# Kernel tuning notes

Measured on AMD Instinct MI355X. Metric: run time of the kernel, lower is better.

The kernel has to match this reference:

```python
import jax, jax.numpy as jnp
import numpy as np

N, E, B, D = 50000, 1600000, 256, 64


def _lin(k, fan_in, fan_out):
    kw, kb = jax.random.split(k)
    bound = 1.0 / np.sqrt(fan_in)
    w = jax.random.uniform(kw, (fan_in, fan_out), jnp.float32, -bound, bound)
    b = jax.random.uniform(kb, (fan_out,), jnp.float32, -bound, bound)
    return w, b


def setup_inputs() -> dict:
    key = jax.random.key(0)
    ks = jax.random.split(key, 16)
    inp = {
        "x": jax.random.normal(ks[0], (N, D), jnp.float32),
        "edge_attr": jax.random.normal(ks[1], (E, D), jnp.float32),
        "u": jax.random.normal(ks[2], (B, D), jnp.float32),
        "edge_index": jax.random.randint(ks[3], (2, E), 0, N, jnp.int32),
        "batch": jnp.sort(jax.random.randint(ks[4], (N,), 0, B, jnp.int32)),
    }
    # three MLPs: edge (in 4D), node (in 3D), global (in 3D); dims [2D, 2D, D]
    specs = [("e", 4 * D), ("n", 3 * D), ("g", 3 * D)]
    ki = 5
    for name, in_dim in specs:
        dims = [in_dim, 2 * D, 2 * D, D]
        for li in range(3):
            w, b = _lin(ks[ki], dims[li], dims[li + 1]); ki += 1
            inp[f"{name}w{li+1}"] = w
            inp[f"{name}b{li+1}"] = b
    return inp


def _mlp(h, w1, b1, w2, b2, w3, b3):
    h = h @ w1 + b1
    h = jax.nn.relu(h) @ w2 + b2
    h = jax.nn.relu(h) @ w3 + b3
    return h


def _scatter_mean(src, idx, num_segments):
    s = jax.ops.segment_sum(src, idx, num_segments=num_segments)
    c = jax.ops.segment_sum(jnp.ones_like(src[:, :1]), idx, num_segments=num_segments)
    return s / jnp.maximum(c, 1.0)


def reference(x, edge_attr, u,
              ew1, eb1, ew2, eb2, ew3, eb3,
              nw1, nb1, nw2, nb2, nw3, nb3,
              gw1, gb1, gw2, gb2, gw3, gb3,
              edge_index, batch):
    row, col = edge_index[0], edge_index[1]
    # edge model: cat[src, dest, edge_attr, u[batch[row]]] -> MLP
    e_in = jnp.concatenate([x[row], x[col], edge_attr, u[batch[row]]], axis=1)  # [E, 4D]
    e = _mlp(e_in, ew1, eb1, ew2, eb2, ew3, eb3)  # [E, D]
    # node model: scatter_mean(edge_attr', row) cat x cat u[batch] -> MLP
    n_agg = _scatter_mean(e, row, x.shape[0])  # [N, D]
    n_in = jnp.concatenate([n_agg, x, u[batch]], axis=1)  # [N, 3D]
    xn = _mlp(n_in, nw1, nb1, nw2, nb2, nw3, nb3)  # [N, D]
    # global model: cat[u, scatter_mean(x', batch), scatter_mean(e', batch[row])]
    edge_mean = _scatter_mean(e, batch[row], u.shape[0])  # [B, D]
    node_mean = _scatter_mean(xn, batch, u.shape[0])  # [B, D]
    g_in = jnp.concatenate([u, node_mean, edge_mean], axis=1)  # [B, 3D]
    un = _mlp(g_in, gw1, gb1, gw2, gb2, gw3, gb3)  # [B, D]
    return xn, e, un
```

## Files before the change

kernel.cpp:

```cpp
#include <hip/hip_runtime.h>

#define NN 50000
#define EE 1600000
#define BBATCH 256
#define DD 64

typedef _Float16 f16;
typedef _Float16 f16x4 __attribute__((ext_vector_type(4)));
typedef _Float16 f16x8 __attribute__((ext_vector_type(8)));
typedef float f32x4 __attribute__((ext_vector_type(4)));

#define MFMA16(a,b,c) __builtin_amdgcn_mfma_f32_16x16x32_f16((a),(b),(c),0,0,0)

constexpr int EW1_RL  = 264;
constexpr int EW1_OFF = 0;
constexpr int EW2_OFF = EW1_OFF + 128 * EW1_RL;
constexpr int EW3_OFF = EW2_OFF + 128 * 136;
constexpr int EH_OFF  = EW3_OFF + 64 * 136;
constexpr int EB_OFF  = EH_OFF + 8 * 16 * 72;
constexpr int ELDS    = EB_OFF + 640;

constexpr int NW1_RL  = 200;
constexpr int NW1_OFF = 0;
constexpr int NW2_OFF = NW1_OFF + 128 * NW1_RL;
constexpr int NW3_OFF = NW2_OFF + 128 * 136;
constexpr int NH_OFF  = NW3_OFF + 64 * 136;
constexpr int NB_OFF  = NH_OFF + 4 * 32 * 136;
constexpr int NLDS    = NB_OFF + 640;

__device__ __forceinline__ f16x8 pack8(const float* __restrict__ p) {
  f32x4 a = *(const f32x4*)p;
  f32x4 b = *(const f32x4*)(p + 4);
  f16x8 r;
  r[0]=(f16)a[0]; r[1]=(f16)a[1]; r[2]=(f16)a[2]; r[3]=(f16)a[3];
  r[4]=(f16)b[0]; r[5]=(f16)b[1]; r[6]=(f16)b[2]; r[7]=(f16)b[3];
  return r;
}
__device__ __forceinline__ f16x8 pack8s(const float* __restrict__ p, float sc) {
  f32x4 a = *(const f32x4*)p;
  f32x4 b = *(const f32x4*)(p + 4);
  a = a * sc; b = b * sc;
  f16x8 r;
  r[0]=(f16)a[0]; r[1]=(f16)a[1]; r[2]=(f16)a[2]; r[3]=(f16)a[3];
  r[4]=(f16)b[0]; r[5]=(f16)b[1]; r[6]=(f16)b[2]; r[7]=(f16)b[3];
  return r;
}
__device__ __forceinline__ f16x8 cvt8(f32x4 a, f32x4 b) {
  f16x8 r;
  r[0]=(f16)a[0]; r[1]=(f16)a[1]; r[2]=(f16)a[2]; r[3]=(f16)a[3];
  r[4]=(f16)b[0]; r[5]=(f16)b[1]; r[6]=(f16)b[2]; r[7]=(f16)b[3];
  return r;
}

template<int KSL, int W1RL, int W1O, int W2O, int W3O>
__device__ __forceinline__ void mlp3_core(f16* __restrict__ sm,
    const float* __restrict__ b1l, const float* __restrict__ b2l,
    const float* __restrict__ b3l,
    const f16x8 (&A1)[2][KSL], const int hb, const int r15, const int g,
    f32x4 (&acc3)[2][4])
{
  #pragma unroll
  for (int hh = 0; hh < 2; ++hh) {
    f32x4 acc[2][4];
    #pragma unroll
    for (int nt = 0; nt < 4; ++nt) {
      const float bv = b1l[(hh*4 + nt)*16 + r15];
      acc[0][nt] = (f32x4){bv, bv, bv, bv};
      acc[1][nt] = acc[0][nt];
    }
    #pragma unroll
    for (int s = 0; s < KSL; ++s) {
      #pragma unroll
      for (int nt = 0; nt < 4; ++nt) {
        const f16x8 bf = *(const f16x8*)&sm[W1O + ((hh*4+nt)*16 + r15) * W1RL + s*32 + g*8];
        acc[0][nt] = MFMA16(A1[0][s], bf, acc[0][nt]);
        acc[1][nt] = MFMA16(A1[1][s], bf, acc[1][nt]);
      }
    }
    #pragma unroll
    for (int mt = 0; mt < 2; ++mt)
      #pragma unroll
      for (int nt = 0; nt < 4; ++nt)
        #pragma unroll
        for (int i = 0; i < 4; ++i)
          sm[hb + (mt*16 + g*4 + i)*136 + (hh*4+nt)*16 + r15] =
              (f16)fmaxf(acc[mt][nt][i], 0.f);
  }

  f16x8 A2[2][4];
  #pragma unroll
  for (int mt = 0; mt < 2; ++mt)
    #pragma unroll
    for (int s = 0; s < 4; ++s)
      A2[mt][s] = *(const f16x8*)&sm[hb + (mt*16 + r15)*136 + s*32 + g*8];

  #pragma unroll
  for (int hh = 0; hh < 2; ++hh) {
    f32x4 acc[2][4];
    #pragma unroll
    for (int nt = 0; nt < 4; ++nt) {
      const float bv = b2l[(hh*4 + nt)*16 + r15];
      acc[0][nt] = (f32x4){bv, bv, bv, bv};
      acc[1][nt] = acc[0][nt];
    }
    #pragma unroll
    for (int s = 0; s < 4; ++s) {
      #pragma unroll
      for (int nt = 0; nt < 4; ++nt) {
        const f16x8 bf = *(const f16x8*)&sm[W2O + ((hh*4+nt)*16 + r15)*136 + s*32 + g*8];
        acc[0][nt] = MFMA16(A2[0][s], bf, acc[0][nt]);
        acc[1][nt] = MFMA16(A2[1][s], bf, acc[1][nt]);
      }
    }
    #pragma unroll
    for (int mt = 0; mt < 2; ++mt)
      #pragma unroll
      for (int nt = 0; nt < 4; ++nt)
        #pragma unroll
        for (int i = 0; i < 4; ++i)
          sm[hb + (mt*16 + g*4 + i)*136 + (hh*4+nt)*16 + r15] =
              (f16)fmaxf(acc[mt][nt][i], 0.f);
  }

  f16x8 A3[2][4];
  #pragma unroll
  for (int mt = 0; mt < 2; ++mt)
    #pragma unroll
    for (int s = 0; s < 4; ++s)
      A3[mt][s] = *(const f16x8*)&sm[hb + (mt*16 + r15)*136 + s*32 + g*8];

  #pragma unroll
  for (int nt = 0; nt < 4; ++nt) {
    const float bv = b3l[nt*16 + r15];
    acc3[0][nt] = (f32x4){bv, bv, bv, bv};
    acc3[1][nt] = acc3[0][nt];
  }
  #pragma unroll
  for (int s = 0; s < 4; ++s) {
    #pragma unroll
    for (int nt = 0; nt < 4; ++nt) {
      const f16x8 bf = *(const f16x8*)&sm[W3O + (nt*16 + r15)*136 + s*32 + g*8];
      acc3[0][nt] = MFMA16(A3[0][s], bf, acc3[0][nt]);
      acc3[1][nt] = MFMA16(A3[1][s], bf, acc3[1][nt]);
    }
  }
}

__global__ void prep_kernel(
    const float* __restrict__ e1, const float* __restrict__ e2, const float* __restrict__ e3,
    const float* __restrict__ n1, const float* __restrict__ n2, const float* __restrict__ n3,
    const float* __restrict__ q1, const float* __restrict__ q2, const float* __restrict__ q3,
    f16* __restrict__ wdst,
    const float* __restrict__ x, const float* __restrict__ u,
    f16* __restrict__ xh, f16* __restrict__ uh,
    const int* __restrict__ ei, int* __restrict__ deg,
    const int* __restrict__ batch, int* __restrict__ bstart)
{
  const int tid = blockIdx.x * 256 + threadIdx.x;

  {
    const int o1=32768,o2=49152,o3=57344,o4=81920,o5=98304,o6=106496,o7=131072,o8=147456,o9=155648;
    if (tid < o9) {
      const float* src; int in, od, rel;
      if      (tid < o1) { src=e1; in=256; od=128; rel=tid;    }
      else if (tid < o2) { src=e2; in=128; od=128; rel=tid-o1; }
      else if (tid < o3) { src=e3; in=128; od=64;  rel=tid-o2; }
      else if (tid < o4) { src=n1; in=192; od=128; rel=tid-o3; }
      else if (tid < o5) { src=n2; in=128; od=128; rel=tid-o4; }
      else if (tid < o6) { src=n3; in=128; od=64;  rel=tid-o5; }
      else if (tid < o7) { src=q1; in=192; od=128; rel=tid-o6; }
      else if (tid < o8) { src=q2; in=128; od=128; rel=tid-o7; }
      else               { src=q3; in=128; od=64;  rel=tid-o8; }
      int o = rel / in, i = rel - o * in;
      wdst[tid] = (f16)src[(size_t)i * od + o];
    }
  }

  if (tid < NN * 64 / 4) {
    f32x4 v = *(const f32x4*)&x[(size_t)tid * 4];
    f16x4 h; h[0]=(f16)v[0]; h[1]=(f16)v[1]; h[2]=(f16)v[2]; h[3]=(f16)v[3];
    *(f16x4*)&xh[(size_t)tid * 4] = h;
  }
  if (tid < BBATCH * 64 / 4) {
    f32x4 v = *(const f32x4*)&u[(size_t)tid * 4];
    f16x4 h; h[0]=(f16)v[0]; h[1]=(f16)v[1]; h[2]=(f16)v[2]; h[3]=(f16)v[3];
    *(f16x4*)&uh[(size_t)tid * 4] = h;
  }

  if (tid < EE) atomicAdd(&deg[ei[tid]], 1);

  if (tid < NN) {
    int b = batch[tid];
    if (tid == 0) { for (int k = 0; k <= b; ++k) bstart[k] = 0; }
    else { int pb = batch[tid - 1]; for (int k = pb + 1; k <= b; ++k) bstart[k] = tid; }
    if (tid == NN - 1) { for (int k = b + 1; k <= BBATCH; ++k) bstart[k] = NN; }
  }
}

__global__ __launch_bounds__(1024) void scan_kernel(const int* __restrict__ deg,
                                                    int* __restrict__ offs,
                                                    int* __restrict__ cursor) {
  const int t = threadIdx.x;
  const int per = (NN + 1023) / 1024;
  const int s0 = t * per;
  int s1 = s0 + per; if (s1 > NN) s1 = NN;
  int sum = 0;
  for (int i = s0; i < s1; ++i) sum += deg[i];
  const int lane = t & 63, wid = t >> 6;
  int v = sum;
  #pragma unroll
  for (int off = 1; off < 64; off <<= 1) {
    int o = __shfl_up(v, off);
    if (lane >= off) v += o;
  }
  __shared__ int wsums[16];
  __shared__ int wexcl[16];
  if (lane == 63) wsums[wid] = v;
  __syncthreads();
  if (t == 0) { int run = 0; for (int k = 0; k < 16; ++k) { wexcl[k] = run; run += wsums[k]; } }
  __syncthreads();
  int run = wexcl[wid] + v - sum;
  for (int i = s0; i < s1; ++i) { int d = deg[i]; offs[i] = run; cursor[i] = run; run += d; }
  if (t == 1023) offs[NN] = run;
}

__global__ void fill_kernel(const int* __restrict__ ei, int* __restrict__ cursor,
                            int* __restrict__ elist) {
  int tid = blockIdx.x * 256 + threadIdx.x;
  if (tid < EE) {
    int r = ei[tid];
    int pos = atomicAdd(&cursor[r], 1);
    elist[pos] = tid;
  }
}

__global__ __launch_bounds__(512, 2) void edge_mlp_kernel(
    const f16* __restrict__ xh, const float* __restrict__ ea,
    const f16* __restrict__ uh, const int* __restrict__ ei,
    const int* __restrict__ batch,
    const f16* __restrict__ w1t, const f16* __restrict__ w2t, const f16* __restrict__ w3t,
    const float* __restrict__ b1, const float* __restrict__ b2, const float* __restrict__ b3,
    float* __restrict__ e_out)
{
  __shared__ __align__(16) f16 sm[ELDS];
  const int t = threadIdx.x;
  for (int c = t; c < 4096; c += 512) { int r = c >> 5, kc = c & 31;
    *(uint4*)&sm[EW1_OFF + r*EW1_RL + kc*8] = *(const uint4*)&w1t[r*256 + kc*8]; }
  for (int c = t; c < 2048; c += 512) { int r = c >> 4, kc = c & 15;
    *(uint4*)&sm[EW2_OFF + r*136 + kc*8] = *(const uint4*)&w2t[r*128 + kc*8]; }
  for (int c = t; c < 1024; c += 512) { int r = c >> 4, kc = c & 15;
    *(uint4*)&sm[EW3_OFF + r*136 + kc*8] = *(const uint4*)&w3t[r*128 + kc*8]; }
  float* bias = (float*)&sm[EB_OFF];
  if (t < 128) { bias[t] = b1[t]; bias[128 + t] = b2[t]; }
  else if (t < 192) { bias[256 + (t - 128)] = b3[t - 128]; }
  __syncthreads();

  const int l = t & 63, w = t >> 6;
  const int r15 = l & 15, g = l >> 4;
  const int hb = EH_OFF + w * (16 * 72);
  const int NT = EE / 256;
  const int stride = gridDim.x;
  const int t0 = blockIdx.x;

  int rC[2], cC[2], bC[2];
  int rN[2], cN[2], bN[2];
  f16x8 Bx[2][6];
  f32x4 Gea[2][2][2];

  auto issueXU = [&](const int (&rr)[2], const int (&cc)[2], const int (&bb)[2]) {
    #pragma unroll
    for (int mt = 0; mt < 2; ++mt) {
      const f16* pr = xh + (size_t)rr[mt] * 64 + g * 8;
      const f16* pc = xh + (size_t)cc[mt] * 64 + g * 8;
      const f16* pu = uh + (size_t)bb[mt] * 64 + g * 8;
      Bx[mt][0] = *(const f16x8*)pr;        Bx[mt][1] = *(const f16x8*)(pr + 32);
      Bx[mt][2] = *(const f16x8*)pc;        Bx[mt][3] = *(const f16x8*)(pc + 32);
      Bx[mt][4] = *(const f16x8*)pu;        Bx[mt][5] = *(const f16x8*)(pu + 32);
    }
  };
  auto issueEA = [&](int tt) {
    #pragma unroll
    for (int mt = 0; mt < 2; ++mt) {
      const float* pe = ea + ((size_t)(tt * 256 + w * 32 + mt * 16 + r15)) * 64 + g * 8;
      #pragma unroll
      for (int ss = 0; ss < 2; ++ss) {
        Gea[mt][ss][0] = *(const f32x4*)(pe + ss * 32);
        Gea[mt][ss][1] = *(const f32x4*)(pe + ss * 32 + 4);
      }
    }
  };

  {
    int rr[2], cc[2], bb[2];
    #pragma unroll
    for (int mt = 0; mt < 2; ++mt) {
      const int eid = t0 * 256 + w * 32 + mt * 16 + r15;
      rr[mt] = ei[eid]; cc[mt] = ei[EE + eid];
    }
    #pragma unroll
    for (int mt = 0; mt < 2; ++mt) bb[mt] = batch[rr[mt]];
    issueXU(rr, cc, bb); issueEA(t0);
    int t1 = t0 + stride; if (t1 >= NT) t1 = t0;
    #pragma unroll
    for (int mt = 0; mt < 2; ++mt) {
      const int eid = t1 * 256 + w * 32 + mt * 16 + r15;
      rC[mt] = ei[eid]; cC[mt] = ei[EE + eid];
    }
    #pragma unroll
    for (int mt = 0; mt < 2; ++mt) bC[mt] = batch[rC[mt]];
  }

  for (int tile = t0; tile < NT; tile += stride) {
    f16x8 A[2][8];
    #pragma unroll
    for (int mt = 0; mt < 2; ++mt) {
      A[mt][0] = Bx[mt][0]; A[mt][1] = Bx[mt][1];
      A[mt][2] = Bx[mt][2]; A[mt][3] = Bx[mt][3];
      A[mt][4] = cvt8(Gea[mt][0][0], Gea[mt][0][1]);
      A[mt][5] = cvt8(Gea[mt][1][0], Gea[mt][1][1]);
      A[mt][6] = Bx[mt][4]; A[mt][7] = Bx[mt][5];
    }

    int t2 = tile + 2 * stride; if (t2 >= NT) t2 = t0;
    #pragma unroll
    for (int mt = 0; mt < 2; ++mt) {
      const int eid = t2 * 256 + w * 32 + mt * 16 + r15;
      rN[mt] = ei[eid]; cN[mt] = ei[EE + eid];
    }

    f32x4 acc1[2][8];
    #pragma unroll
    for (int a = 0; a < 8; ++a) {
      const f32x4 bv = *(const f32x4*)&bias[a*16 + g*4];
      acc1[0][a] = bv; acc1[1][a] = bv;
    }
    #pragma unroll
    for (int s = 0; s < 8; ++s)
      #pragma unroll
      for (int a = 0; a < 8; ++a) {
        const f16x8 wf = *(const f16x8*)&sm[EW1_OFF + (a*16 + r15)*EW1_RL + s*32 + g*8];
        acc1[0][a] = MFMA16(wf, A[0][s], acc1[0][a]);
        acc1[1][a] = MFMA16(wf, A[1][s], acc1[1][a]);
      }

    #pragma unroll
    for (int mt = 0; mt < 2; ++mt) bN[mt] = batch[rN[mt]];

    f16x8 B2[2][4];
    #pragma unroll
    for (int mt = 0; mt < 2; ++mt)
      #pragma unroll
      for (int hh = 0; hh < 2; ++hh) {
        #pragma unroll
        for (int ap = 0; ap < 4; ++ap) {
          const f32x4 v = acc1[mt][hh*4 + ap];
          f16x4 hv;
          hv[0]=(f16)fmaxf(v[0],0.f); hv[1]=(f16)fmaxf(v[1],0.f);
          hv[2]=(f16)fmaxf(v[2],0.f); hv[3]=(f16)fmaxf(v[3],0.f);
          *(f16x4*)&sm[hb + r15*72 + ap*16 + g*4] = hv;
        }
        #pragma unroll
        for (int sl = 0; sl < 2; ++sl)
          B2[mt][hh*2 + sl] = *(const f16x8*)&sm[hb + r15*72 + sl*32 + g*8];
      }

    int t1 = tile + stride; if (t1 >= NT) t1 = t0;
    issueXU(rC, cC, bC);

    f32x4 acc2[2][8];
    #pragma unroll
    for (int a = 0; a < 8; ++a) {
      const f32x4 bv = *(const f32x4*)&bias[128 + a*16 + g*4];
      acc2[0][a] = bv; acc2[1][a] = bv;
    }
    #pragma unroll
    for (int s = 0; s < 4; ++s)
      #pragma unroll
      for (int a = 0; a < 8; ++a) {
        const f16x8 wf = *(const f16x8*)&sm[EW2_OFF + (a*16 + r15)*136 + s*32 + g*8];
        acc2[0][a] = MFMA16(wf, B2[0][s], acc2[0][a]);
        acc2[1][a] = MFMA16(wf, B2[1][s], acc2[1][a]);
      }

    f16x8 B3[2][4];
    #pragma unroll
    for (int mt = 0; mt < 2; ++mt)
      #pragma unroll
      for (int hh = 0; hh < 2; ++hh) {
        #pragma unroll
        for (int ap = 0; ap < 4; ++ap) {
          const f32x4 v = acc2[mt][hh*4 + ap];
          f16x4 hv;
          hv[0]=(f16)fmaxf(v[0],0.f); hv[1]=(f16)fmaxf(v[1],0.f);
          hv[2]=(f16)fmaxf(v[2],0.f); hv[3]=(f16)fmaxf(v[3],0.f);
          *(f16x4*)&sm[hb + r15*72 + ap*16 + g*4] = hv;
        }
        #pragma unroll
        for (int sl = 0; sl < 2; ++sl)
          B3[mt][hh*2 + sl] = *(const f16x8*)&sm[hb + r15*72 + sl*32 + g*8];
      }

    issueEA(t1);

    f32x4 acc3[2][4];
    #pragma unroll
    for (int a = 0; a < 4; ++a) {
      const f32x4 bv = *(const f32x4*)&bias[256 + a*16 + g*4];
      acc3[0][a] = bv; acc3[1][a] = bv;
    }
    #pragma unroll
    for (int s = 0; s < 4; ++s)
      #pragma unroll
      for (int a = 0; a < 4; ++a) {
        const f16x8 wf = *(const f16x8*)&sm[EW3_OFF + (a*16 + r15)*136 + s*32 + g*8];
        acc3[0][a] = MFMA16(wf, B3[0][s], acc3[0][a]);
        acc3[1][a] = MFMA16(wf, B3[1][s], acc3[1][a]);
      }

    const int base = tile * 256 + w * 32;
    #pragma unroll
    for (int mt = 0; mt < 2; ++mt) {
      const int m = base + mt * 16 + r15;
      #pragma unroll
      for (int a = 0; a < 4; ++a)
        *(f32x4*)&e_out[(size_t)m * 64 + a*16 + g*4] = acc3[mt][a];
    }

    #pragma unroll
    for (int mt = 0; mt < 2; ++mt) { rC[mt] = rN[mt]; cC[mt] = cN[mt]; bC[mt] = bN[mt]; }
  }
}

__global__ void nsum_kernel(const float* __restrict__ e_src, const int* __restrict__ offs,
                            const int* __restrict__ elist, float* __restrict__ n_sum) {
  const int l = threadIdx.x & 63;
  const int wid = (blockIdx.x * blockDim.x + threadIdx.x) >> 6;
  const int nw = (gridDim.x * blockDim.x) >> 6;
  for (int node = wid; node < NN; node += nw) {
    const int s = offs[node], e = offs[node + 1];
    float acc = 0.f;
    int j = s;
    for (; j + 16 <= e; j += 16) {
      float v[16];
      #pragma unroll
      for (int k = 0; k < 16; ++k) v[k] = e_src[(size_t)elist[j + k] * 64 + l];
      float s0 = ((v[0]+v[1])+(v[2]+v[3])) + ((v[4]+v[5])+(v[6]+v[7]));
      float s1 = ((v[8]+v[9])+(v[10]+v[11])) + ((v[12]+v[13])+(v[14]+v[15]));
      acc += s0 + s1;
    }
    for (; j + 4 <= e; j += 4) {
      float v0 = e_src[(size_t)elist[j]   * 64 + l];
      float v1 = e_src[(size_t)elist[j+1] * 64 + l];
      float v2 = e_src[(size_t)elist[j+2] * 64 + l];
      float v3 = e_src[(size_t)elist[j+3] * 64 + l];
      acc += (v0 + v1) + (v2 + v3);
    }
    for (; j < e; ++j) acc += e_src[(size_t)elist[j] * 64 + l];
    n_sum[(size_t)node * 64 + l] = acc;
  }
}

__global__ __launch_bounds__(256, 1) void node_mlp_kernel(
    const float* __restrict__ x, const float* __restrict__ u,
    const int* __restrict__ batch, const float* __restrict__ n_sum,
    const int* __restrict__ deg,
    const f16* __restrict__ w1t, const f16* __restrict__ w2t, const f16* __restrict__ w3t,
    const float* __restrict__ b1, const float* __restrict__ b2, const float* __restrict__ b3,
    float* __restrict__ xn_out)
{
  __shared__ __align__(16) f16 sm[NLDS];
  const int t = threadIdx.x;
  for (int c = t; c < 3072; c += 256) { int r = c / 24, kc = c - r * 24;
    *(uint4*)&sm[NW1_OFF + r*NW1_RL + kc*8] = *(const uint4*)&w1t[r*192 + kc*8]; }
  for (int c = t; c < 2048; c += 256) { int r = c >> 4, kc = c & 15;
    *(uint4*)&sm[NW2_OFF + r*136 + kc*8] = *(const uint4*)&w2t[r*128 + kc*8]; }
  for (int c = t; c < 1024; c += 256) { int r = c >> 4, kc = c & 15;
    *(uint4*)&sm[NW3_OFF + r*136 + kc*8] = *(const uint4*)&w3t[r*128 + kc*8]; }
  float* bias = (float*)&sm[NB_OFF];
  if (t < 128) { bias[t] = b1[t]; bias[128 + t] = b2[t]; }
  if (t < 64)  { bias[256 + t] = b3[t]; }
  __syncthreads();

  const int l = t & 63, w = t >> 6;
  const int r15 = l & 15, g = l >> 4;
  const int hb = NH_OFF + w * (32 * 136);
  const int NTT = (NN + 127) / 128;

  for (int tile = blockIdx.x; tile < NTT; tile += gridDim.x) {
    const int base = tile * 128 + w * 32;
    f16x8 A1[2][6];
    #pragma unroll
    for (int mt = 0; mt < 2; ++mt) {
      int raw = base + mt * 16 + r15;
      int node = raw < NN ? raw : NN - 1;
      float inv = 1.0f / fmaxf((float)deg[node], 1.0f);
      const float* sA = n_sum + (size_t)node * 64;
      const float* sB = x + (size_t)node * 64;
      const float* sC = u + (size_t)batch[node] * 64;
      #pragma unroll
      for (int s = 0; s < 6; ++s) {
        const int off = (s & 1) * 32 + g * 8;
        if (s < 2)      A1[mt][s] = pack8s(sA + off, inv);
        else if (s < 4) A1[mt][s] = pack8(sB + off);
        else            A1[mt][s] = pack8(sC + off);
      }
    }
    f32x4 acc3[2][4];
    mlp3_core<6, NW1_RL, NW1_OFF, NW2_OFF, NW3_OFF>(sm, bias, bias + 128, bias + 256,
                                                    A1, hb, r15, g, acc3);
    #pragma unroll
    for (int mt = 0; mt < 2; ++mt)
      #pragma unroll
      for (int nt = 0; nt < 4; ++nt)
        #pragma unroll
        for (int i = 0; i < 4; ++i) {
          const int m = base + mt * 16 + g * 4 + i;
          if (m < NN) xn_out[(size_t)m * 64 + nt * 16 + r15] = acc3[mt][nt][i];
        }
  }
}

__global__ void batch_sum_kernel(const float* __restrict__ xn, const float* __restrict__ n_sum,
                                 const int* __restrict__ deg, const int* __restrict__ bstart,
                                 float* __restrict__ nbsum, float* __restrict__ ebsum,
                                 int* __restrict__ ncnt, int* __restrict__ ecnt) {
  __shared__ float red0[256];
  __shared__ float red1[256];
  __shared__ int   redi[256];
  const int b = blockIdx.x;
  const int s = bstart[b], e = bstart[b + 1];
  const int t = threadIdx.x, c = t & 63, j0 = t >> 6;
  float xs = 0.f, ns = 0.f; int dc = 0;
  for (int j = s + j0; j < e; j += 4) {
    xs += xn[(size_t)j * 64 + c];
    ns += n_sum[(size_t)j * 64 + c];
    if (c == 0) dc += deg[j];
  }
  red0[t] = xs; red1[t] = ns; redi[t] = dc;
  __syncthreads();
  if (t < 128) { red0[t] += red0[t + 128]; red1[t] += red1[t + 128]; redi[t] += redi[t + 128]; }
  __syncthreads();
  if (t < 64) {
    float a0 = red0[t] + red0[t + 64];
    float a1 = red1[t] + red1[t + 64];
    nbsum[b * 64 + t] = a0;
    ebsum[b * 64 + t] = a1;
    if (t == 0) { ncnt[b] = e - s; ecnt[b] = redi[0] + redi[64]; }
  }
}

__global__ __launch_bounds__(256, 1) void global_mlp_kernel(
    const float* __restrict__ u, const float* __restrict__ nbsum,
    const float* __restrict__ ebsum, const int* __restrict__ ncnt,
    const int* __restrict__ ecnt,
    const f16* __restrict__ w1t, const f16* __restrict__ w2t, const f16* __restrict__ w3t,
    const float* __restrict__ b1, const float* __restrict__ b2, const float* __restrict__ b3,
    float* __restrict__ un_out)
{
  __shared__ __align__(16) f16 sm[NLDS];
  const int t = threadIdx.x;
  for (int c = t; c < 3072; c += 256) { int r = c / 24, kc = c - r * 24;
    *(uint4*)&sm[NW1_OFF + r*NW1_RL + kc*8] = *(const uint4*)&w1t[r*192 + kc*8]; }
  for (int c = t; c < 2048; c += 256) { int r = c >> 4, kc = c & 15;
    *(uint4*)&sm[NW2_OFF + r*136 + kc*8] = *(const uint4*)&w2t[r*128 + kc*8]; }
  for (int c = t; c < 1024; c += 256) { int r = c >> 4, kc = c & 15;
    *(uint4*)&sm[NW3_OFF + r*136 + kc*8] = *(const uint4*)&w3t[r*128 + kc*8]; }
  float* bias = (float*)&sm[NB_OFF];
  if (t < 128) { bias[t] = b1[t]; bias[128 + t] = b2[t]; }
  if (t < 64)  { bias[256 + t] = b3[t]; }
  __syncthreads();

  const int l = t & 63, w = t >> 6;
  const int r15 = l & 15, g = l >> 4;
  const int hb = NH_OFF + w * (32 * 136);
  const int base = blockIdx.x * 128 + w * 32;

  f16x8 A1[2][6];
  #pragma unroll
  for (int mt = 0; mt < 2; ++mt) {
    const int r = base + mt * 16 + r15;
    const float invn = 1.0f / fmaxf((float)ncnt[r], 1.0f);
    const float inve = 1.0f / fmaxf((float)ecnt[r], 1.0f);
    const float* sA = u + (size_t)r * 64;
    const float* sB = nbsum + (size_t)r * 64;
    const float* sC = ebsum + (size_t)r * 64;
    #pragma unroll
    for (int s = 0; s < 6; ++s) {
      const int off = (s & 1) * 32 + g * 8;
      if (s < 2)      A1[mt][s] = pack8(sA + off);
      else if (s < 4) A1[mt][s] = pack8s(sB + off, invn);
      else            A1[mt][s] = pack8s(sC + off, inve);
    }
  }
  f32x4 acc3[2][4];
  mlp3_core<6, NW1_RL, NW1_OFF, NW2_OFF, NW3_OFF>(sm, bias, bias + 128, bias + 256,
                                                  A1, hb, r15, g, acc3);
  #pragma unroll
  for (int mt = 0; mt < 2; ++mt)
    #pragma unroll
    for (int nt = 0; nt < 4; ++nt)
      #pragma unroll
      for (int i = 0; i < 4; ++i) {
        const int m = base + mt * 16 + g * 4 + i;
        un_out[(size_t)m * 64 + nt * 16 + r15] = acc3[mt][nt][i];
      }
}

extern "C" void kernel_launch(void* const* d_in, const int* in_sizes, int n_in,
                              void* d_out, int out_size, void* d_ws, size_t ws_size,
                              hipStream_t stream)
{
  (void)in_sizes; (void)n_in; (void)out_size; (void)ws_size;
  const float* x     = (const float*)d_in[0];
  const float* ea    = (const float*)d_in[1];
  const float* u     = (const float*)d_in[2];
  const int*   ei    = (const int*)d_in[3];
  const int*   batch = (const int*)d_in[4];
  const float* ew1 = (const float*)d_in[5];  const float* eb1 = (const float*)d_in[6];
  const float* ew2 = (const float*)d_in[7];  const float* eb2 = (const float*)d_in[8];
  const float* ew3 = (const float*)d_in[9];  const float* eb3 = (const float*)d_in[10];
  const float* nw1 = (const float*)d_in[11]; const float* nb1 = (const float*)d_in[12];
  const float* nw2 = (const float*)d_in[13]; const float* nb2 = (const float*)d_in[14];
  const float* nw3 = (const float*)d_in[15]; const float* nb3 = (const float*)d_in[16];
  const float* gw1 = (const float*)d_in[17]; const float* gb1 = (const float*)d_in[18];
  const float* gw2 = (const float*)d_in[19]; const float* gb2 = (const float*)d_in[20];
  const float* gw3 = (const float*)d_in[21]; const float* gb3 = (const float*)d_in[22];

  float* xn_out = (float*)d_out;
  float* e_out  = xn_out + (size_t)NN * DD;
  float* un_out = e_out + (size_t)EE * DD;

  char* p = (char*)d_ws;
  auto alloc = [&](size_t bytes) -> void* {
    void* r = (void*)p; p += (bytes + 255) & ~(size_t)255; return r;
  };
  f16* wtE1 = (f16*)alloc(256 * 128 * 2);
  f16* wtE2 = (f16*)alloc(128 * 128 * 2);
  f16* wtE3 = (f16*)alloc(128 * 64 * 2);
  f16* wtN1 = (f16*)alloc(192 * 128 * 2);
  f16* wtN2 = (f16*)alloc(128 * 128 * 2);
  f16* wtN3 = (f16*)alloc(128 * 64 * 2);
  f16* wtG1 = (f16*)alloc(192 * 128 * 2);
  f16* wtG2 = (f16*)alloc(128 * 128 * 2);
  f16* wtG3 = (f16*)alloc(128 * 64 * 2);
  int* deg    = (int*)alloc((size_t)NN * 4);
  int* offs   = (int*)alloc((size_t)(NN + 1) * 4);
  int* cursor = (int*)alloc((size_t)NN * 4);
  int* elist  = (int*)alloc((size_t)EE * 4);
  int* bstart = (int*)alloc((size_t)(BBATCH + 1) * 4);
  float* nbsum = (float*)alloc((size_t)BBATCH * 64 * 4);
  float* ebsum = (float*)alloc((size_t)BBATCH * 64 * 4);
  int* ncnt = (int*)alloc((size_t)BBATCH * 4);
  int* ecnt = (int*)alloc((size_t)BBATCH * 4);
  float* n_sum = (float*)alloc((size_t)NN * 64 * 4);
  f16* xh = (f16*)alloc((size_t)NN * 64 * 2);
  f16* uh = (f16*)alloc((size_t)BBATCH * 64 * 2);

  hipMemsetAsync(deg, 0, (size_t)NN * 4, stream);
  prep_kernel<<<dim3(6250), dim3(256), 0, stream>>>(
      ew1, ew2, ew3, nw1, nw2, nw3, gw1, gw2, gw3, wtE1,
      x, u, xh, uh, ei, deg, batch, bstart);
  scan_kernel<<<dim3(1), dim3(1024), 0, stream>>>(deg, offs, cursor);
  fill_kernel<<<dim3(6250), dim3(256), 0, stream>>>(ei, cursor, elist);

  edge_mlp_kernel<<<dim3(256), dim3(512), 0, stream>>>(
      xh, ea, uh, ei, batch, wtE1, wtE2, wtE3, eb1, eb2, eb3, e_out);

  nsum_kernel<<<dim3(4096), dim3(256), 0, stream>>>(e_out, offs, elist, n_sum);

  node_mlp_kernel<<<dim3(256), dim3(256), 0, stream>>>(
      x, u, batch, n_sum, deg, wtN1, wtN2, wtN3, nb1, nb2, nb3, xn_out);

  batch_sum_kernel<<<dim3(BBATCH), dim3(256), 0, stream>>>(
      xn_out, n_sum, deg, bstart, nbsum, ebsum, ncnt, ecnt);

  global_mlp_kernel<<<dim3(2), dim3(256), 0, stream>>>(
      u, nbsum, ebsum, ncnt, ecnt, wtG1, wtG2, wtG3, gb1, gb2, gb3, un_out);
}
```

Before: 731.3 us.

## Replace CSR gather segment-sum with direct float atomic scatter of edge outputs

Drops the single-block scan and the fill kernel that built a row-sorted edge list, and instead scatters each edge's output row into the node sums with float atomicAdd. This removes the serial 1024-thread scan, the atomic-cursor fill and the indirect gather. In exchange it issues 1.6M×64 float atomics to random node rows, which can be slower than the gather, and it makes the summation order nondeterministic. It also adds a memset of the node-sum buffer.

```diff
diff --git a/kernel.cpp b/kernel.cpp
--- a/kernel.cpp
+++ b/kernel.cpp
@@ -194,43 +194,6 @@
     if (tid == 0) { for (int k = 0; k <= b; ++k) bstart[k] = 0; }
     else { int pb = batch[tid - 1]; for (int k = pb + 1; k <= b; ++k) bstart[k] = tid; }
     if (tid == NN - 1) { for (int k = b + 1; k <= BBATCH; ++k) bstart[k] = NN; }
-  }
-}
-
-__global__ __launch_bounds__(1024) void scan_kernel(const int* __restrict__ deg,
-                                                    int* __restrict__ offs,
-                                                    int* __restrict__ cursor) {
-  const int t = threadIdx.x;
-  const int per = (NN + 1023) / 1024;
-  const int s0 = t * per;
-  int s1 = s0 + per; if (s1 > NN) s1 = NN;
-  int sum = 0;
-  for (int i = s0; i < s1; ++i) sum += deg[i];
-  const int lane = t & 63, wid = t >> 6;
-  int v = sum;
-  #pragma unroll
-  for (int off = 1; off < 64; off <<= 1) {
-    int o = __shfl_up(v, off);
-    if (lane >= off) v += o;
-  }
-  __shared__ int wsums[16];
-  __shared__ int wexcl[16];
-  if (lane == 63) wsums[wid] = v;
-  __syncthreads();
-  if (t == 0) { int run = 0; for (int k = 0; k < 16; ++k) { wexcl[k] = run; run += wsums[k]; } }
-  __syncthreads();
-  int run = wexcl[wid] + v - sum;
-  for (int i = s0; i < s1; ++i) { int d = deg[i]; offs[i] = run; cursor[i] = run; run += d; }
-  if (t == 1023) offs[NN] = run;
-}
-
-__global__ void fill_kernel(const int* __restrict__ ei, int* __restrict__ cursor,
-                            int* __restrict__ elist) {
-  int tid = blockIdx.x * 256 + threadIdx.x;
-  if (tid < EE) {
-    int r = ei[tid];
-    int pos = atomicAdd(&cursor[r], 1);
-    elist[pos] = tid;
   }
 }
 
@@ -431,32 +394,21 @@
   }
 }
 
-__global__ void nsum_kernel(const float* __restrict__ e_src, const int* __restrict__ offs,
-                            const int* __restrict__ elist, float* __restrict__ n_sum) {
+__global__ void escatter_kernel(const float* __restrict__ e_src, const int* __restrict__ ei,
+                                float* __restrict__ n_sum) {
   const int l = threadIdx.x & 63;
   const int wid = (blockIdx.x * blockDim.x + threadIdx.x) >> 6;
   const int nw = (gridDim.x * blockDim.x) >> 6;
-  for (int node = wid; node < NN; node += nw) {
-    const int s = offs[node], e = offs[node + 1];
-    float acc = 0.f;
-    int j = s;
-    for (; j + 16 <= e; j += 16) {
-      float v[16];
-      #pragma unroll
-      for (int k = 0; k < 16; ++k) v[k] = e_src[(size_t)elist[j + k] * 64 + l];
-      float s0 = ((v[0]+v[1])+(v[2]+v[3])) + ((v[4]+v[5])+(v[6]+v[7]));
-      float s1 = ((v[8]+v[9])+(v[10]+v[11])) + ((v[12]+v[13])+(v[14]+v[15]));
-      acc += s0 + s1;
-    }
-    for (; j + 4 <= e; j += 4) {
-      float v0 = e_src[(size_t)elist[j]   * 64 + l];
-      float v1 = e_src[(size_t)elist[j+1] * 64 + l];
-      float v2 = e_src[(size_t)elist[j+2] * 64 + l];
-      float v3 = e_src[(size_t)elist[j+3] * 64 + l];
-      acc += (v0 + v1) + (v2 + v3);
-    }
-    for (; j < e; ++j) acc += e_src[(size_t)elist[j] * 64 + l];
-    n_sum[(size_t)node * 64 + l] = acc;
+  for (int base = wid * 4; base < EE; base += nw * 4) {
+    float v[4]; int r[4];
+    #pragma unroll
+    for (int k = 0; k < 4; ++k) {
+      v[k] = e_src[(size_t)(base + k) * 64 + l];
+      r[k] = ei[base + k];
+    }
+    #pragma unroll
+    for (int k = 0; k < 4; ++k)
+      atomicAdd(&n_sum[(size_t)r[k] * 64 + l], v[k]);
   }
 }
 
@@ -644,9 +596,6 @@
   f16* wtG2 = (f16*)alloc(128 * 128 * 2);
   f16* wtG3 = (f16*)alloc(128 * 64 * 2);
   int* deg    = (int*)alloc((size_t)NN * 4);
-  int* offs   = (int*)alloc((size_t)(NN + 1) * 4);
-  int* cursor = (int*)alloc((size_t)NN * 4);
-  int* elist  = (int*)alloc((size_t)EE * 4);
   int* bstart = (int*)alloc((size_t)(BBATCH + 1) * 4);
   float* nbsum = (float*)alloc((size_t)BBATCH * 64 * 4);
   float* ebsum = (float*)alloc((size_t)BBATCH * 64 * 4);
@@ -657,16 +606,15 @@
   f16* uh = (f16*)alloc((size_t)BBATCH * 64 * 2);
 
   hipMemsetAsync(deg, 0, (size_t)NN * 4, stream);
+  hipMemsetAsync(n_sum, 0, (size_t)NN * 64 * 4, stream);
   prep_kernel<<<dim3(6250), dim3(256), 0, stream>>>(
       ew1, ew2, ew3, nw1, nw2, nw3, gw1, gw2, gw3, wtE1,
       x, u, xh, uh, ei, deg, batch, bstart);
-  scan_kernel<<<dim3(1), dim3(1024), 0, stream>>>(deg, offs, cursor);
-  fill_kernel<<<dim3(6250), dim3(256), 0, stream>>>(ei, cursor, elist);
 
   edge_mlp_kernel<<<dim3(256), dim3(512), 0, stream>>>(
       xh, ea, uh, ei, batch, wtE1, wtE2, wtE3, eb1, eb2, eb3, e_out);
 
-  nsum_kernel<<<dim3(4096), dim3(256), 0, stream>>>(e_out, offs, elist, n_sum);
+  escatter_kernel<<<dim3(4096), dim3(256), 0, stream>>>(e_out, ei, n_sum);
 
   node_mlp_kernel<<<dim3(256), dim3(256), 0, stream>>>(
       x, u, batch, n_sum, deg, wtN1, wtN2, wtN3, nb1, nb2, nb3, xn_out);
```

Result: no change. 727.8 us (-0.5%).
